# Kernel optimization log

Measured on AMD Instinct MI355X. Metric: run time of the kernel, lower is better.

## Reference

```python
import jax, jax.numpy as jnp
import numpy as np

B, R, SR, K, F = 1, 2048, 24, 8, 32
DIST_FREQ = 2   # dist_xyz_freq -> PE dim 2*2*3 = 12
VIEW_FREQ = 4   # num_viewdir_freqs -> PE dim 2*4*3 = 24


def pe(x, n_freqs):
    # positional encoding: concat sin/cos of x * 2^i, flattened over last dim
    fb = (2.0 ** jnp.arange(n_freqs)).astype(x.dtype)          # [L]
    xb = x[..., None] * fb                                      # [..., 3, L]
    enc = jnp.concatenate([jnp.sin(xb), jnp.cos(xb)], axis=-1)  # [..., 3, 2L]
    return enc.reshape(*x.shape[:-1], -1)                       # [..., 3*2L]


def setup_inputs() -> dict:
    key = jax.random.key(0)
    ks = jax.random.split(key, 12)
    s = 0.1  # small init scale for weights
    return {
        'sampled_embedding': jax.random.normal(ks[0], (B, R, SR, K, F), jnp.float32),
        'dists': jax.random.normal(ks[1], (B, R, SR, K, 3), jnp.float32) * 0.1,
        'viewdirs': jax.random.normal(ks[2], (B, R, SR, 3), jnp.float32),
        'pnt_mask': jax.random.randint(ks[3], (B, R, SR, K), 0, 2, jnp.int32),
        'w1': jax.random.normal(ks[4], (F + 2 * DIST_FREQ * 3, 256), jnp.float32) * s,
        'b1': jnp.zeros((256,), jnp.float32),
        'w2': jax.random.normal(ks[5], (256, 256), jnp.float32) * s,
        'b2': jnp.zeros((256,), jnp.float32),
        'wa1': jax.random.normal(ks[6], (256, 256), jnp.float32) * s,
        'ba1': jnp.zeros((256,), jnp.float32),
        'wa2': jax.random.normal(ks[7], (256, 1), jnp.float32) * s,
        'ba2': jnp.zeros((1,), jnp.float32),
        'wc1': jax.random.normal(ks[8], (256 + 2 * VIEW_FREQ * 3, 256), jnp.float32) * s,
        'bc1': jnp.zeros((256,), jnp.float32),
        'wc2': jax.random.normal(ks[9], (256, 3), jnp.float32) * s,
        'bc2': jnp.zeros((3,), jnp.float32),
    }


def reference(sampled_embedding, dists, viewdirs, pnt_mask,
              w1, b1, w2, b2, wa1, ba1, wa2, ba2, wc1, bc1, wc2, bc2):
    mask = pnt_mask.astype(sampled_embedding.dtype)             # [B,R,SR,K]

    # quadric distance kernel -> normalized neighbor weights
    d2 = jnp.sum(dists * dists, axis=-1)                        # [B,R,SR,K]
    w = 1.0 / jnp.clip(d2, 1e-8)
    w = w * mask
    w = w / jnp.clip(jnp.sum(w, axis=-1, keepdims=True), 1e-8)  # agg_weight_norm

    # per-neighbor feature MLP (block1): feat ++ PE(dist_xyz) -> 256 -> 256
    feat_in = jnp.concatenate([sampled_embedding, pe(dists, DIST_FREQ)], axis=-1)
    h = jax.nn.relu(feat_in @ w1 + b1)
    h = jax.nn.relu(h @ w2 + b2)                                # [B,R,SR,K,256]

    # distance-weighted aggregation over neighbors (apply_pnt_mask folded into w)
    agg = jnp.einsum('brsk,brskc->brsc', w, h)                  # [B,R,SR,256]

    # alpha branch + raw2out_density (act_super: softplus(raw - 1))
    ah = jax.nn.relu(agg @ wa1 + ba1)
    density = jax.nn.softplus(ah @ wa2 + ba2 - 1.0)             # [B,R,SR,1]

    # color branch + raw2out_color (widened sigmoid)
    cin = jnp.concatenate([agg, pe(viewdirs, VIEW_FREQ)], axis=-1)
    ch = jax.nn.relu(cin @ wc1 + bc1)
    color = jax.nn.sigmoid(ch @ wc2 + bc2) * (1.0 + 2e-3) - 1e-3  # [B,R,SR,3]

    return jnp.concatenate([density, color], axis=-1)           # [B,R,SR,4]
```

## Files before the change

### kernel.cpp

```cpp
#include <hip/hip_runtime.h>

typedef unsigned short ushort_t;
typedef __bf16 bf16x8 __attribute__((ext_vector_type(8)));
typedef float f32x4 __attribute__((ext_vector_type(4)));

#define NPTS   49152
#define KNBR   8
#define PTS_A  16
#define NBLK_A (NPTS / PTS_A)
#define PTS_B  32
#define NBLK_B (NPTS / PTS_B)

#define W1S_OFF   0
#define W2S_OFF   16384
#define WA1S_OFF  81920
#define WC1S_OFF  147456
#define WA2S_OFF  221184
#define WC2S_OFF  225280
#define WS_WEIGHT 229376
#define AGG_OFF   229376

__device__ __forceinline__ float b2f(ushort_t u) {
    return __builtin_bit_cast(float, ((unsigned)u) << 16);
}
__device__ __forceinline__ ushort_t f2b(float f) {
    unsigned x = __builtin_bit_cast(unsigned, f);
    unsigned r = x + 0x7fffu + ((x >> 16) & 1u);
    return (ushort_t)(r >> 16);
}
__device__ __forceinline__ ushort_t f2bc(float f) {
    unsigned x = __builtin_bit_cast(unsigned, f);
    return (ushort_t)((x + 0x8000u) >> 16);
}

__global__ __launch_bounds__(256) void prep_swizzle(
    const float* __restrict__ w1, const float* __restrict__ w2,
    const float* __restrict__ wa1, const float* __restrict__ wc1,
    const float* __restrict__ wa2, const float* __restrict__ wc2,
    ushort_t* __restrict__ ws)
{
    int idx = blockIdx.x * 256 + threadIdx.x;
    if (idx >= WS_WEIGHT) return;

    if (idx >= WA2S_OFF) {
        int off2 = idx - WA2S_OFF;
        int mat = off2 >> 12;
        int off = off2 & 4095;
        int kb = off >> 7, rem = off & 127;
        int n = rem >> 3, j = rem & 7;
        int k = kb * 8 + j;
        float v = 0.f;
        if (mat == 0) { if (n == 0) v = wa2[k]; }
        else          { if (n < 3)  v = wc2[k * 3 + n]; }
        ws[idx] = f2b(v);
        return;
    }

    const float* src; int off, srcK, base;
    if (idx < W2S_OFF)        { src = w1;  base = W1S_OFF;  off = idx - W1S_OFF;  srcK = 44;  }
    else if (idx < WA1S_OFF)  { src = w2;  base = W2S_OFF;  off = idx - W2S_OFF;  srcK = 256; }
    else if (idx < WC1S_OFF)  { src = wa1; base = WA1S_OFF; off = idx - WA1S_OFF; srcK = 256; }
    else                      { src = wc1; base = WC1S_OFF; off = idx - WC1S_OFF; srcK = 280; }
    int kb  = off >> 11;
    int rem = off & 2047;
    int j = rem >> 8;
    int n = rem & 255;
    int k = kb * 8 + j;
    float v = (k < srcK) ? src[k * 256 + n] : 0.f;
    ws[base + kb * 2048 + n * 8 + j] = f2b(v);
}

__global__ __launch_bounds__(512, 4) void pa_mlp(
    const float* __restrict__ emb, const float* __restrict__ dists,
    const int* __restrict__ mask,  const float* __restrict__ b1,
    const float* __restrict__ b2,  const ushort_t* __restrict__ ws,
    ushort_t* __restrict__ aggg)
{
    __shared__ __align__(16) ushort_t uH1[128 * 264];
    __shared__ __align__(16) float sWraw[128];
    __shared__ __align__(16) float sWn[128];
    ushort_t (*sFeat)[72] = (ushort_t(*)[72])uH1;
    ushort_t (*sH1)[264]  = (ushort_t(*)[264])uH1;

    const int tid  = threadIdx.x;
    const int lane = tid & 63;
    const int wv   = tid >> 6;
    const int wm   = wv >> 2;
    const int wn   = wv & 3;
    const int n0   = lane & 15;
    const int quad = lane >> 4;
    const int pb   = blockIdx.x * PTS_A;
    const int rowB = wm * 64;
    const int colB = wn * 64;

    {
        int g0 = blockIdx.x * 4096 + tid * 8;
        int r = tid >> 2, c8 = (tid & 3) * 8;
        float4 f0 = *(const float4*)(emb + g0);
        float4 f1 = *(const float4*)(emb + g0 + 4);
        ushort_t v8[8];
        v8[0] = f2bc(f0.x); v8[1] = f2bc(f0.y); v8[2] = f2bc(f0.z); v8[3] = f2bc(f0.w);
        v8[4] = f2bc(f1.x); v8[5] = f2bc(f1.y); v8[6] = f2bc(f1.z); v8[7] = f2bc(f1.w);
        *(uint4*)&sFeat[r][c8] = *(uint4*)v8;
    }
    if (tid < 128) {
        int gr = pb * KNBR + tid;
        float x = dists[gr * 3 + 0];
        float y = dists[gr * 3 + 1];
        float z = dists[gr * 3 + 2];
        float d2 = x * x + y * y + z * z;
        sWraw[tid] = (float)mask[gr] / fmaxf(d2, 1e-8f);
        float xs[3] = {x, y, z};
        #pragma unroll
        for (int d = 0; d < 3; d++) {
            #pragma unroll
            for (int l = 0; l < 2; l++) {
                float ang = xs[d] * (float)(1 << l);
                sFeat[tid][32 + d * 4 + l]     = f2bc(__sinf(ang));
                sFeat[tid][32 + d * 4 + 2 + l] = f2bc(__cosf(ang));
            }
        }
        #pragma unroll
        for (int c = 44; c < 64; c++) sFeat[tid][c] = 0;
    }
    __syncthreads();
    if (tid < 128) {
        int lp = tid >> 3;
        float s = 0.f;
        #pragma unroll
        for (int k = 0; k < 8; k++) s += sWraw[lp * 8 + k];
        sWn[tid] = sWraw[tid] / fmaxf(s, 1e-8f);
    }

    f32x4 acc[16];
    #pragma unroll
    for (int i = 0; i < 16; i++) acc[i] = (f32x4){0.f, 0.f, 0.f, 0.f};

    #pragma unroll
    for (int ki = 0; ki < 2; ki++) {
        bf16x8 a[4];
        #pragma unroll
        for (int mt = 0; mt < 4; mt++)
            a[mt] = *(const bf16x8*)&sFeat[rowB + mt * 16 + n0][ki * 32 + quad * 8];
        const ushort_t* bp = ws + W1S_OFF + ki * 8192 + quad * 2048 + (colB + n0) * 8;
        #pragma unroll
        for (int nt = 0; nt < 4; nt++) {
            bf16x8 b = *(const bf16x8*)(bp + nt * 128);
            #pragma unroll
            for (int mt = 0; mt < 4; mt++)
                acc[mt * 4 + nt] = __builtin_amdgcn_mfma_f32_16x16x32_bf16(a[mt], b, acc[mt * 4 + nt], 0, 0, 0);
        }
    }
    __syncthreads();

    {
        #pragma unroll
        for (int nt = 0; nt < 4; nt++) {
            int col = colB + nt * 16 + n0;
            float bias = b1[col];
            #pragma unroll
            for (int mt = 0; mt < 4; mt++)
                #pragma unroll
                for (int r = 0; r < 4; r++)
                    sH1[rowB + mt * 16 + quad * 4 + r][col] = f2bc(fmaxf(acc[mt * 4 + nt][r] + bias, 0.f));
        }
    }
    __syncthreads();

    #pragma unroll
    for (int i = 0; i < 16; i++) acc[i] = (f32x4){0.f, 0.f, 0.f, 0.f};
    #pragma unroll
    for (int ki = 0; ki < 8; ki++) {
        bf16x8 a[4];
        #pragma unroll
        for (int mt = 0; mt < 4; mt++)
            a[mt] = *(const bf16x8*)&sH1[rowB + mt * 16 + n0][ki * 32 + quad * 8];
        const ushort_t* bp = ws + W2S_OFF + ki * 8192 + quad * 2048 + (colB + n0) * 8;
        #pragma unroll
        for (int nt = 0; nt < 4; nt++) {
            bf16x8 b = *(const bf16x8*)(bp + nt * 128);
            #pragma unroll
            for (int mt = 0; mt < 4; mt++)
                acc[mt * 4 + nt] = __builtin_amdgcn_mfma_f32_16x16x32_bf16(a[mt], b, acc[mt * 4 + nt], 0, 0, 0);
        }
    }
    {
        #pragma unroll
        for (int mt = 0; mt < 4; mt++) {
            f32x4 wn4 = *(const f32x4*)&sWn[rowB + mt * 16 + quad * 4];
            #pragma unroll
            for (int nt = 0; nt < 4; nt++) {
                int col = colB + nt * 16 + n0;
                float bias = b2[col];
                float s = fmaxf(acc[mt * 4 + nt][0] + bias, 0.f) * wn4[0]
                        + fmaxf(acc[mt * 4 + nt][1] + bias, 0.f) * wn4[1]
                        + fmaxf(acc[mt * 4 + nt][2] + bias, 0.f) * wn4[2]
                        + fmaxf(acc[mt * 4 + nt][3] + bias, 0.f) * wn4[3];
                s += __shfl_xor(s, 16);
                if ((quad & 1) == 0) {
                    int pt = pb + 8 * wm + 2 * mt + (quad >> 1);
                    aggg[(size_t)pt * 256 + col] = f2bc(s);
                }
            }
        }
    }
}

__global__ __launch_bounds__(256) void pa_branch(
    const float* __restrict__ vdirs,
    const float* __restrict__ ba1v, const float* __restrict__ ba2v,
    const float* __restrict__ bc1v, const float* __restrict__ bc2v,
    const ushort_t* __restrict__ ws, const ushort_t* __restrict__ aggg,
    float* __restrict__ out)
{
    __shared__ __align__(16) ushort_t reg1[32 * 296];
    __shared__ __align__(16) ushort_t reg2[32 * 264];
    ushort_t (*sCin)[296] = (ushort_t(*)[296])reg1;
    ushort_t (*sAh)[264]  = (ushort_t(*)[264])reg1;
    ushort_t (*sCh)[264]  = (ushort_t(*)[264])reg2;

    const int tid  = threadIdx.x;
    const int lane = tid & 63;
    const int wv   = tid >> 6;
    const int n0   = lane & 15;
    const int quad = lane >> 4;
    const int pb   = blockIdx.x * PTS_B;
    const int colB = wv * 64;

    #pragma unroll
    for (int it = 0; it < 4; it++) {
        int idx = (tid + it * 256) * 8;
        uint4 v = *(const uint4*)(aggg + (size_t)pb * 256 + idx);
        *(uint4*)&sCin[idx >> 8][idx & 255] = v;
    }
    #pragma unroll
    for (int it = 0; it < 3; it++) {
        int t = tid + it * 256;
        int p = t / 24, j = t % 24;
        int d = j >> 3, jj = j & 7, l = jj & 3, isc = jj >> 2;
        float ang = vdirs[(pb + p) * 3 + d] * (float)(1 << l);
        sCin[p][256 + j] = f2bc(isc ? __cosf(ang) : __sinf(ang));
    }
    sCin[tid >> 3][280 + (tid & 7)] = 0;
    __syncthreads();

    f32x4 accA[8], accC[8];
    #pragma unroll
    for (int i = 0; i < 8; i++) { accA[i] = (f32x4){0.f, 0.f, 0.f, 0.f}; accC[i] = accA[i]; }

    #pragma unroll
    for (int ki = 0; ki < 8; ki++) {
        bf16x8 a0 = *(const bf16x8*)&sCin[n0][ki * 32 + quad * 8];
        bf16x8 a1 = *(const bf16x8*)&sCin[16 + n0][ki * 32 + quad * 8];
        const ushort_t* bp = ws + WA1S_OFF + ki * 8192 + quad * 2048 + (colB + n0) * 8;
        #pragma unroll
        for (int nt = 0; nt < 4; nt++) {
            bf16x8 b = *(const bf16x8*)(bp + nt * 128);
            accA[nt]     = __builtin_amdgcn_mfma_f32_16x16x32_bf16(a0, b, accA[nt], 0, 0, 0);
            accA[4 + nt] = __builtin_amdgcn_mfma_f32_16x16x32_bf16(a1, b, accA[4 + nt], 0, 0, 0);
        }
    }
    #pragma unroll
    for (int ki = 0; ki < 9; ki++) {
        bf16x8 a0 = *(const bf16x8*)&sCin[n0][ki * 32 + quad * 8];
        bf16x8 a1 = *(const bf16x8*)&sCin[16 + n0][ki * 32 + quad * 8];
        const ushort_t* bp = ws + WC1S_OFF + ki * 8192 + quad * 2048 + (colB + n0) * 8;
        #pragma unroll
        for (int nt = 0; nt < 4; nt++) {
            bf16x8 b = *(const bf16x8*)(bp + nt * 128);
            accC[nt]     = __builtin_amdgcn_mfma_f32_16x16x32_bf16(a0, b, accC[nt], 0, 0, 0);
            accC[4 + nt] = __builtin_amdgcn_mfma_f32_16x16x32_bf16(a1, b, accC[4 + nt], 0, 0, 0);
        }
    }
    __syncthreads();

    #pragma unroll
    for (int nt = 0; nt < 4; nt++) {
        int col = colB + nt * 16 + n0;
        float biasA = ba1v[col];
        float biasC = bc1v[col];
        #pragma unroll
        for (int mt = 0; mt < 2; mt++)
            #pragma unroll
            for (int r = 0; r < 4; r++) {
                int row = mt * 16 + quad * 4 + r;
                sAh[row][col] = f2bc(fmaxf(accA[mt * 4 + nt][r] + biasA, 0.f));
                sCh[row][col] = f2bc(fmaxf(accC[mt * 4 + nt][r] + biasC, 0.f));
            }
    }
    __syncthreads();

    {
        const int isColor = wv >> 1;
        const int baseM   = (wv & 1) * 16;
        const ushort_t* A = isColor ? &sCh[0][0] : &sAh[0][0];
        const ushort_t* B = ws + (isColor ? WC2S_OFF : WA2S_OFF);
        f32x4 acc4 = (f32x4){0.f, 0.f, 0.f, 0.f};
        #pragma unroll
        for (int ki = 0; ki < 8; ki++) {
            bf16x8 a = *(const bf16x8*)(A + (baseM + n0) * 264 + ki * 32 + quad * 8);
            bf16x8 b = *(const bf16x8*)(B + ki * 512 + quad * 128 + n0 * 8);
            acc4 = __builtin_amdgcn_mfma_f32_16x16x32_bf16(a, b, acc4, 0, 0, 0);
        }
        if (!isColor) {
            if (n0 == 0) {
                float ba2s = ba2v[0];
                #pragma unroll
                for (int r = 0; r < 4; r++) {
                    int gp = pb + baseM + quad * 4 + r;
                    float yv = acc4[r] + ba2s - 1.0f;
                    out[(size_t)gp * 4] = (yv > 20.f) ? yv : log1pf(expf(yv));
                }
            }
        } else {
            if (n0 < 3) {
                float bc2s = bc2v[n0];
                #pragma unroll
                for (int r = 0; r < 4; r++) {
                    int gp = pb + baseM + quad * 4 + r;
                    float sig = 1.f / (1.f + expf(-(acc4[r] + bc2s)));
                    out[(size_t)gp * 4 + 1 + n0] = sig * (1.0f + 2e-3f) - 1e-3f;
                }
            }
        }
    }
}

extern "C" void kernel_launch(void* const* d_in, const int* in_sizes, int n_in,
                              void* d_out, int out_size, void* d_ws, size_t ws_size,
                              hipStream_t stream) {
    const float* emb   = (const float*)d_in[0];
    const float* dists = (const float*)d_in[1];
    const float* vdir  = (const float*)d_in[2];
    const int*   mask  = (const int*)d_in[3];
    const float* w1    = (const float*)d_in[4];
    const float* b1    = (const float*)d_in[5];
    const float* w2    = (const float*)d_in[6];
    const float* b2    = (const float*)d_in[7];
    const float* wa1   = (const float*)d_in[8];
    const float* ba1   = (const float*)d_in[9];
    const float* wa2   = (const float*)d_in[10];
    const float* ba2   = (const float*)d_in[11];
    const float* wc1   = (const float*)d_in[12];
    const float* bc1   = (const float*)d_in[13];
    const float* wc2   = (const float*)d_in[14];
    const float* bc2   = (const float*)d_in[15];
    ushort_t* ws  = (ushort_t*)d_ws;
    float*    out = (float*)d_out;

    prep_swizzle<<<dim3((WS_WEIGHT + 255) / 256), dim3(256), 0, stream>>>(
        w1, w2, wa1, wc1, wa2, wc2, ws);
    pa_mlp<<<dim3(NBLK_A), dim3(512), 0, stream>>>(
        emb, dists, mask, b1, b2, ws, ws + AGG_OFF);
    pa_branch<<<dim3(NBLK_B), dim3(256), 0, stream>>>(
        vdir, ba1, ba2, bc1, bc2, ws, ws + AGG_OFF, out);
}
```

Baseline: 200.3 us.

## Switch MLP matmuls to 32x32x16 MFMA tiles with W2 register prefetch

Both kernels move from 16x16x32 bf16 MFMA to 32x32x16 bf16 MFMA. This halves the number of A/B fragment loads per output and cuts instruction count, and the fragment indexing and epilogue row mapping are rewritten to match the 32x32 accumulator layout. The W2 loop in pa_mlp also double-buffers the global weight fragments in registers so the next k-step's loads overlap the current MFMAs. The trade-off is larger accumulator vectors and more live registers, which could pressure occupancy under launch_bounds(512,4). The weight layout assumption (ki*4096 + hi*2048 stride) must match the preprocessed weight packing.

```diff
diff --git a/kernel.cpp b/kernel.cpp
--- a/kernel.cpp
+++ b/kernel.cpp
@@ -3,6 +3,7 @@
 typedef unsigned short ushort_t;
 typedef __bf16 bf16x8 __attribute__((ext_vector_type(8)));
 typedef float f32x4 __attribute__((ext_vector_type(4)));
+typedef float f32x16 __attribute__((ext_vector_type(16)));
 
 #define NPTS   49152
 #define KNBR   8
@@ -87,8 +88,8 @@
     const int wv   = tid >> 6;
     const int wm   = wv >> 2;
     const int wn   = wv & 3;
-    const int n0   = lane & 15;
-    const int quad = lane >> 4;
+    const int l31  = lane & 31;
+    const int hi   = lane >> 5;
     const int pb   = blockIdx.x * PTS_A;
     const int rowB = wm * 64;
     const int colB = wn * 64;
@@ -132,74 +133,84 @@
         sWn[tid] = sWraw[tid] / fmaxf(s, 1e-8f);
     }
 
-    f32x4 acc[16];
-    #pragma unroll
-    for (int i = 0; i < 16; i++) acc[i] = (f32x4){0.f, 0.f, 0.f, 0.f};
-
-    #pragma unroll
-    for (int ki = 0; ki < 2; ki++) {
-        bf16x8 a[4];
-        #pragma unroll
-        for (int mt = 0; mt < 4; mt++)
-            a[mt] = *(const bf16x8*)&sFeat[rowB + mt * 16 + n0][ki * 32 + quad * 8];
-        const ushort_t* bp = ws + W1S_OFF + ki * 8192 + quad * 2048 + (colB + n0) * 8;
-        #pragma unroll
-        for (int nt = 0; nt < 4; nt++) {
-            bf16x8 b = *(const bf16x8*)(bp + nt * 128);
-            #pragma unroll
-            for (int mt = 0; mt < 4; mt++)
-                acc[mt * 4 + nt] = __builtin_amdgcn_mfma_f32_16x16x32_bf16(a[mt], b, acc[mt * 4 + nt], 0, 0, 0);
-        }
-    }
-    __syncthreads();
-
-    {
-        #pragma unroll
-        for (int nt = 0; nt < 4; nt++) {
-            int col = colB + nt * 16 + n0;
+    f32x16 acc[4];
+    #pragma unroll
+    for (int i = 0; i < 4; i++) acc[i] = (f32x16)(0.f);
+
+    #pragma unroll
+    for (int ki = 0; ki < 4; ki++) {
+        bf16x8 a0 = *(const bf16x8*)&sFeat[rowB + l31][ki * 16 + hi * 8];
+        bf16x8 a1 = *(const bf16x8*)&sFeat[rowB + 32 + l31][ki * 16 + hi * 8];
+        const ushort_t* bp = ws + W1S_OFF + ki * 4096 + hi * 2048 + (colB + l31) * 8;
+        bf16x8 b0 = *(const bf16x8*)(bp);
+        bf16x8 b1f = *(const bf16x8*)(bp + 256);
+        acc[0] = __builtin_amdgcn_mfma_f32_32x32x16_bf16(a0, b0,  acc[0], 0, 0, 0);
+        acc[1] = __builtin_amdgcn_mfma_f32_32x32x16_bf16(a0, b1f, acc[1], 0, 0, 0);
+        acc[2] = __builtin_amdgcn_mfma_f32_32x32x16_bf16(a1, b0,  acc[2], 0, 0, 0);
+        acc[3] = __builtin_amdgcn_mfma_f32_32x32x16_bf16(a1, b1f, acc[3], 0, 0, 0);
+    }
+    __syncthreads();
+
+    {
+        #pragma unroll
+        for (int nt = 0; nt < 2; nt++) {
+            int col = colB + nt * 32 + l31;
             float bias = b1[col];
             #pragma unroll
-            for (int mt = 0; mt < 4; mt++)
+            for (int mt = 0; mt < 2; mt++) {
                 #pragma unroll
-                for (int r = 0; r < 4; r++)
-                    sH1[rowB + mt * 16 + quad * 4 + r][col] = f2bc(fmaxf(acc[mt * 4 + nt][r] + bias, 0.f));
-        }
-    }
-    __syncthreads();
-
-    #pragma unroll
-    for (int i = 0; i < 16; i++) acc[i] = (f32x4){0.f, 0.f, 0.f, 0.f};
-    #pragma unroll
-    for (int ki = 0; ki < 8; ki++) {
-        bf16x8 a[4];
-        #pragma unroll
-        for (int mt = 0; mt < 4; mt++)
-            a[mt] = *(const bf16x8*)&sH1[rowB + mt * 16 + n0][ki * 32 + quad * 8];
-        const ushort_t* bp = ws + W2S_OFF + ki * 8192 + quad * 2048 + (colB + n0) * 8;
-        #pragma unroll
-        for (int nt = 0; nt < 4; nt++) {
-            bf16x8 b = *(const bf16x8*)(bp + nt * 128);
+                for (int reg = 0; reg < 16; reg++) {
+                    int row = rowB + mt * 32 + (reg & 3) + 8 * (reg >> 2) + 4 * hi;
+                    sH1[row][col] = f2bc(fmaxf(acc[mt * 2 + nt][reg] + bias, 0.f));
+                }
+            }
+        }
+    }
+    __syncthreads();
+
+    #pragma unroll
+    for (int i = 0; i < 4; i++) acc[i] = (f32x16)(0.f);
+    {
+        const ushort_t* w2base = ws + W2S_OFF + hi * 2048 + (colB + l31) * 8;
+        bf16x8 bc0 = *(const bf16x8*)(w2base);
+        bf16x8 bc1 = *(const bf16x8*)(w2base + 256);
+        #pragma unroll
+        for (int ki = 0; ki < 16; ki++) {
+            bf16x8 bn0, bn1;
+            if (ki < 15) {
+                const ushort_t* p = w2base + (ki + 1) * 4096;
+                bn0 = *(const bf16x8*)(p);
+                bn1 = *(const bf16x8*)(p + 256);
+            }
+            bf16x8 a0 = *(const bf16x8*)&sH1[rowB + l31][ki * 16 + hi * 8];
+            bf16x8 a1 = *(const bf16x8*)&sH1[rowB + 32 + l31][ki * 16 + hi * 8];
+            acc[0] = __builtin_amdgcn_mfma_f32_32x32x16_bf16(a0, bc0, acc[0], 0, 0, 0);
+            acc[1] = __builtin_amdgcn_mfma_f32_32x32x16_bf16(a0, bc1, acc[1], 0, 0, 0);
+            acc[2] = __builtin_amdgcn_mfma_f32_32x32x16_bf16(a1, bc0, acc[2], 0, 0, 0);
+            acc[3] = __builtin_amdgcn_mfma_f32_32x32x16_bf16(a1, bc1, acc[3], 0, 0, 0);
+            bc0 = bn0; bc1 = bn1;
+        }
+    }
+    {
+        #pragma unroll
+        for (int mt = 0; mt < 2; mt++) {
             #pragma unroll
-            for (int mt = 0; mt < 4; mt++)
-                acc[mt * 4 + nt] = __builtin_amdgcn_mfma_f32_16x16x32_bf16(a[mt], b, acc[mt * 4 + nt], 0, 0, 0);
-        }
-    }
-    {
-        #pragma unroll
-        for (int mt = 0; mt < 4; mt++) {
-            f32x4 wn4 = *(const f32x4*)&sWn[rowB + mt * 16 + quad * 4];
-            #pragma unroll
-            for (int nt = 0; nt < 4; nt++) {
-                int col = colB + nt * 16 + n0;
+            for (int nt = 0; nt < 2; nt++) {
+                int col = colB + nt * 32 + l31;
                 float bias = b2[col];
-                float s = fmaxf(acc[mt * 4 + nt][0] + bias, 0.f) * wn4[0]
-                        + fmaxf(acc[mt * 4 + nt][1] + bias, 0.f) * wn4[1]
-                        + fmaxf(acc[mt * 4 + nt][2] + bias, 0.f) * wn4[2]
-                        + fmaxf(acc[mt * 4 + nt][3] + bias, 0.f) * wn4[3];
-                s += __shfl_xor(s, 16);
-                if ((quad & 1) == 0) {
-                    int pt = pb + 8 * wm + 2 * mt + (quad >> 1);
-                    aggg[(size_t)pt * 256 + col] = f2bc(s);
+                f32x16 v = acc[mt * 2 + nt];
+                #pragma unroll
+                for (int q = 0; q < 4; q++) {
+                    f32x4 wn4 = *(const f32x4*)&sWn[rowB + mt * 32 + q * 8 + 4 * hi];
+                    float s = fmaxf(v[q * 4 + 0] + bias, 0.f) * wn4[0]
+                            + fmaxf(v[q * 4 + 1] + bias, 0.f) * wn4[1]
+                            + fmaxf(v[q * 4 + 2] + bias, 0.f) * wn4[2]
+                            + fmaxf(v[q * 4 + 3] + bias, 0.f) * wn4[3];
+                    s += __shfl_xor(s, 32);
+                    if (hi == 0) {
+                        int pt = pb + wm * 8 + mt * 4 + q;
+                        aggg[(size_t)pt * 256 + col] = f2bc(s);
+                    }
                 }
             }
         }
@@ -222,6 +233,8 @@
     const int tid  = threadIdx.x;
     const int lane = tid & 63;
     const int wv   = tid >> 6;
+    const int l31  = lane & 31;
+    const int hi   = lane >> 5;
     const int n0   = lane & 15;
     const int quad = lane >> 4;
     const int pb   = blockIdx.x * PTS_B;
@@ -244,49 +257,43 @@
     sCin[tid >> 3][280 + (tid & 7)] = 0;
     __syncthreads();
 
-    f32x4 accA[8], accC[8];
-    #pragma unroll
-    for (int i = 0; i < 8; i++) { accA[i] = (f32x4){0.f, 0.f, 0.f, 0.f}; accC[i] = accA[i]; }
-
-    #pragma unroll
-    for (int ki = 0; ki < 8; ki++) {
-        bf16x8 a0 = *(const bf16x8*)&sCin[n0][ki * 32 + quad * 8];
-        bf16x8 a1 = *(const bf16x8*)&sCin[16 + n0][ki * 32 + quad * 8];
-        const ushort_t* bp = ws + WA1S_OFF + ki * 8192 + quad * 2048 + (colB + n0) * 8;
-        #pragma unroll
-        for (int nt = 0; nt < 4; nt++) {
-            bf16x8 b = *(const bf16x8*)(bp + nt * 128);
-            accA[nt]     = __builtin_amdgcn_mfma_f32_16x16x32_bf16(a0, b, accA[nt], 0, 0, 0);
-            accA[4 + nt] = __builtin_amdgcn_mfma_f32_16x16x32_bf16(a1, b, accA[4 + nt], 0, 0, 0);
-        }
-    }
-    #pragma unroll
-    for (int ki = 0; ki < 9; ki++) {
-        bf16x8 a0 = *(const bf16x8*)&sCin[n0][ki * 32 + quad * 8];
-        bf16x8 a1 = *(const bf16x8*)&sCin[16 + n0][ki * 32 + quad * 8];
-        const ushort_t* bp = ws + WC1S_OFF + ki * 8192 + quad * 2048 + (colB + n0) * 8;
-        #pragma unroll
-        for (int nt = 0; nt < 4; nt++) {
-            bf16x8 b = *(const bf16x8*)(bp + nt * 128);
-            accC[nt]     = __builtin_amdgcn_mfma_f32_16x16x32_bf16(a0, b, accC[nt], 0, 0, 0);
-            accC[4 + nt] = __builtin_amdgcn_mfma_f32_16x16x32_bf16(a1, b, accC[4 + nt], 0, 0, 0);
-        }
-    }
-    __syncthreads();
-
-    #pragma unroll
-    for (int nt = 0; nt < 4; nt++) {
-        int col = colB + nt * 16 + n0;
-        float biasA = ba1v[col];
-        float biasC = bc1v[col];
-        #pragma unroll
-        for (int mt = 0; mt < 2; mt++)
+    f32x16 accA[2], accC[2];
+    #pragma unroll
+    for (int i = 0; i < 2; i++) { accA[i] = (f32x16)(0.f); accC[i] = (f32x16)(0.f); }
+
+    #pragma unroll
+    for (int ki = 0; ki < 16; ki++) {
+        bf16x8 a0 = *(const bf16x8*)&sCin[l31][ki * 16 + hi * 8];
+        const ushort_t* bp = ws + WA1S_OFF + ki * 4096 + hi * 2048 + (colB + l31) * 8;
+        bf16x8 b0 = *(const bf16x8*)(bp);
+        bf16x8 b1f = *(const bf16x8*)(bp + 256);
+        accA[0] = __builtin_amdgcn_mfma_f32_32x32x16_bf16(a0, b0,  accA[0], 0, 0, 0);
+        accA[1] = __builtin_amdgcn_mfma_f32_32x32x16_bf16(a0, b1f, accA[1], 0, 0, 0);
+    }
+    #pragma unroll
+    for (int ki = 0; ki < 18; ki++) {
+        bf16x8 a0 = *(const bf16x8*)&sCin[l31][ki * 16 + hi * 8];
+        const ushort_t* bp = ws + WC1S_OFF + ki * 4096 + hi * 2048 + (colB + l31) * 8;
+        bf16x8 b0 = *(const bf16x8*)(bp);
+        bf16x8 b1f = *(const bf16x8*)(bp + 256);
+        accC[0] = __builtin_amdgcn_mfma_f32_32x32x16_bf16(a0, b0,  accC[0], 0, 0, 0);
+        accC[1] = __builtin_amdgcn_mfma_f32_32x32x16_bf16(a0, b1f, accC[1], 0, 0, 0);
+    }
+    __syncthreads();
+
+    {
+        #pragma unroll
+        for (int nt = 0; nt < 2; nt++) {
+            int col = colB + nt * 32 + l31;
+            float biasA = ba1v[col];
+            float biasC = bc1v[col];
             #pragma unroll
-            for (int r = 0; r < 4; r++) {
-                int row = mt * 16 + quad * 4 + r;
-                sAh[row][col] = f2bc(fmaxf(accA[mt * 4 + nt][r] + biasA, 0.f));
-                sCh[row][col] = f2bc(fmaxf(accC[mt * 4 + nt][r] + biasC, 0.f));
-            }
+            for (int reg = 0; reg < 16; reg++) {
+                int row = (reg & 3) + 8 * (reg >> 2) + 4 * hi;
+                sAh[row][col] = f2bc(fmaxf(accA[nt][reg] + biasA, 0.f));
+                sCh[row][col] = f2bc(fmaxf(accC[nt][reg] + biasC, 0.f));
+            }
+        }
     }
     __syncthreads();
 
```

New measurement: 203.8 us. About the same (+1.8%).

## Fuse alpha/color branch MLP into aggregation kernel via shared memory

Applied to the files above, without the earlier changes.

Merges the branch kernel into the per-neighbor MLP kernel so each 16-point block computes aggregated features into LDS and then runs the alpha and color heads directly. This removes the global write and re-read of the bf16 aggregation buffer and one kernel launch. In exchange, each block now does its branch GEMMs with M=16 rows, so branch weights are reloaded from global/L2 per 16 points instead of per 32. It also adds LDS use and extra barriers, which may reduce occupancy.

```diff
diff --git a/kernel.cpp b/kernel.cpp
--- a/kernel.cpp
+++ b/kernel.cpp
@@ -8,8 +8,6 @@
 #define KNBR   8
 #define PTS_A  16
 #define NBLK_A (NPTS / PTS_A)
-#define PTS_B  32
-#define NBLK_B (NPTS / PTS_B)
 
 #define W1S_OFF   0
 #define W2S_OFF   16384
@@ -18,7 +16,6 @@
 #define WA2S_OFF  221184
 #define WC2S_OFF  225280
 #define WS_WEIGHT 229376
-#define AGG_OFF   229376
 
 __device__ __forceinline__ float b2f(ushort_t u) {
     return __builtin_bit_cast(float, ((unsigned)u) << 16);
@@ -72,15 +69,21 @@
 
 __global__ __launch_bounds__(512, 4) void pa_mlp(
     const float* __restrict__ emb, const float* __restrict__ dists,
-    const int* __restrict__ mask,  const float* __restrict__ b1,
-    const float* __restrict__ b2,  const ushort_t* __restrict__ ws,
-    ushort_t* __restrict__ aggg)
+    const int* __restrict__ mask,  const float* __restrict__ vdirs,
+    const float* __restrict__ b1,  const float* __restrict__ b2,
+    const float* __restrict__ ba1v, const float* __restrict__ ba2v,
+    const float* __restrict__ bc1v, const float* __restrict__ bc2v,
+    const ushort_t* __restrict__ ws, float* __restrict__ out)
 {
     __shared__ __align__(16) ushort_t uH1[128 * 264];
     __shared__ __align__(16) float sWraw[128];
     __shared__ __align__(16) float sWn[128];
+    __shared__ __align__(16) ushort_t uCin[16 * 296];
     ushort_t (*sFeat)[72] = (ushort_t(*)[72])uH1;
     ushort_t (*sH1)[264]  = (ushort_t(*)[264])uH1;
+    ushort_t (*sAh)[264]  = (ushort_t(*)[264])uH1;
+    ushort_t (*sCh)[264]  = (ushort_t(*)[264])(uH1 + 16 * 264);
+    ushort_t (*sCi)[296]  = (ushort_t(*)[296])uCin;
 
     const int tid  = threadIdx.x;
     const int lane = tid & 63;
@@ -122,6 +125,13 @@
         }
         #pragma unroll
         for (int c = 44; c < 64; c++) sFeat[tid][c] = 0;
+        sCi[tid >> 3][280 + (tid & 7)] = 0;
+    }
+    if (tid < 384) {
+        int p = tid / 24, j = tid % 24;
+        int d = j >> 3, jj = j & 7, l = jj & 3, isc = jj >> 2;
+        float ang = vdirs[(pb + p) * 3 + d] * (float)(1 << l);
+        sCi[p][256 + j] = f2bc(isc ? __cosf(ang) : __sinf(ang));
     }
     __syncthreads();
     if (tid < 128) {
@@ -198,107 +208,61 @@
                         + fmaxf(acc[mt * 4 + nt][3] + bias, 0.f) * wn4[3];
                 s += __shfl_xor(s, 16);
                 if ((quad & 1) == 0) {
-                    int pt = pb + 8 * wm + 2 * mt + (quad >> 1);
-                    aggg[(size_t)pt * 256 + col] = f2bc(s);
+                    int ptl = 8 * wm + 2 * mt + (quad >> 1);
+                    sCi[ptl][col] = f2bc(s);
                 }
             }
         }
     }
-}
-
-__global__ __launch_bounds__(256) void pa_branch(
-    const float* __restrict__ vdirs,
-    const float* __restrict__ ba1v, const float* __restrict__ ba2v,
-    const float* __restrict__ bc1v, const float* __restrict__ bc2v,
-    const ushort_t* __restrict__ ws, const ushort_t* __restrict__ aggg,
-    float* __restrict__ out)
-{
-    __shared__ __align__(16) ushort_t reg1[32 * 296];
-    __shared__ __align__(16) ushort_t reg2[32 * 264];
-    ushort_t (*sCin)[296] = (ushort_t(*)[296])reg1;
-    ushort_t (*sAh)[264]  = (ushort_t(*)[264])reg1;
-    ushort_t (*sCh)[264]  = (ushort_t(*)[264])reg2;
-
-    const int tid  = threadIdx.x;
-    const int lane = tid & 63;
-    const int wv   = tid >> 6;
-    const int n0   = lane & 15;
-    const int quad = lane >> 4;
-    const int pb   = blockIdx.x * PTS_B;
-    const int colB = wv * 64;
-
-    #pragma unroll
-    for (int it = 0; it < 4; it++) {
-        int idx = (tid + it * 256) * 8;
-        uint4 v = *(const uint4*)(aggg + (size_t)pb * 256 + idx);
-        *(uint4*)&sCin[idx >> 8][idx & 255] = v;
-    }
-    #pragma unroll
-    for (int it = 0; it < 3; it++) {
-        int t = tid + it * 256;
-        int p = t / 24, j = t % 24;
-        int d = j >> 3, jj = j & 7, l = jj & 3, isc = jj >> 2;
-        float ang = vdirs[(pb + p) * 3 + d] * (float)(1 << l);
-        sCin[p][256 + j] = f2bc(isc ? __cosf(ang) : __sinf(ang));
-    }
-    sCin[tid >> 3][280 + (tid & 7)] = 0;
-    __syncthreads();
-
-    f32x4 accA[8], accC[8];
-    #pragma unroll
-    for (int i = 0; i < 8; i++) { accA[i] = (f32x4){0.f, 0.f, 0.f, 0.f}; accC[i] = accA[i]; }
-
-    #pragma unroll
-    for (int ki = 0; ki < 8; ki++) {
-        bf16x8 a0 = *(const bf16x8*)&sCin[n0][ki * 32 + quad * 8];
-        bf16x8 a1 = *(const bf16x8*)&sCin[16 + n0][ki * 32 + quad * 8];
-        const ushort_t* bp = ws + WA1S_OFF + ki * 8192 + quad * 2048 + (colB + n0) * 8;
+    __syncthreads();
+
+    {
+        const int isColor = wv >> 2;
+        const int colBb   = (wv & 3) * 64;
+        const ushort_t* Wb = ws + (isColor ? WC1S_OFF : WA1S_OFF);
+        const float* biasv = isColor ? bc1v : ba1v;
+        f32x4 accB[4];
+        #pragma unroll
+        for (int i = 0; i < 4; i++) accB[i] = (f32x4){0.f, 0.f, 0.f, 0.f};
+        #pragma unroll
+        for (int ki = 0; ki < 8; ki++) {
+            bf16x8 a0 = *(const bf16x8*)&sCi[n0][ki * 32 + quad * 8];
+            const ushort_t* bp = Wb + ki * 8192 + quad * 2048 + (colBb + n0) * 8;
+            #pragma unroll
+            for (int nt = 0; nt < 4; nt++) {
+                bf16x8 b = *(const bf16x8*)(bp + nt * 128);
+                accB[nt] = __builtin_amdgcn_mfma_f32_16x16x32_bf16(a0, b, accB[nt], 0, 0, 0);
+            }
+        }
+        if (isColor) {
+            bf16x8 a0 = *(const bf16x8*)&sCi[n0][8 * 32 + quad * 8];
+            const ushort_t* bp = Wb + 8 * 8192 + quad * 2048 + (colBb + n0) * 8;
+            #pragma unroll
+            for (int nt = 0; nt < 4; nt++) {
+                bf16x8 b = *(const bf16x8*)(bp + nt * 128);
+                accB[nt] = __builtin_amdgcn_mfma_f32_16x16x32_bf16(a0, b, accB[nt], 0, 0, 0);
+            }
+        }
+        ushort_t (*sOut)[264] = isColor ? sCh : sAh;
         #pragma unroll
         for (int nt = 0; nt < 4; nt++) {
-            bf16x8 b = *(const bf16x8*)(bp + nt * 128);
-            accA[nt]     = __builtin_amdgcn_mfma_f32_16x16x32_bf16(a0, b, accA[nt], 0, 0, 0);
-            accA[4 + nt] = __builtin_amdgcn_mfma_f32_16x16x32_bf16(a1, b, accA[4 + nt], 0, 0, 0);
-        }
-    }
-    #pragma unroll
-    for (int ki = 0; ki < 9; ki++) {
-        bf16x8 a0 = *(const bf16x8*)&sCin[n0][ki * 32 + quad * 8];
-        bf16x8 a1 = *(const bf16x8*)&sCin[16 + n0][ki * 32 + quad * 8];
-        const ushort_t* bp = ws + WC1S_OFF + ki * 8192 + quad * 2048 + (colB + n0) * 8;
-        #pragma unroll
-        for (int nt = 0; nt < 4; nt++) {
-            bf16x8 b = *(const bf16x8*)(bp + nt * 128);
-            accC[nt]     = __builtin_amdgcn_mfma_f32_16x16x32_bf16(a0, b, accC[nt], 0, 0, 0);
-            accC[4 + nt] = __builtin_amdgcn_mfma_f32_16x16x32_bf16(a1, b, accC[4 + nt], 0, 0, 0);
-        }
-    }
-    __syncthreads();
-
-    #pragma unroll
-    for (int nt = 0; nt < 4; nt++) {
-        int col = colB + nt * 16 + n0;
-        float biasA = ba1v[col];
-        float biasC = bc1v[col];
-        #pragma unroll
-        for (int mt = 0; mt < 2; mt++)
-            #pragma unroll
-            for (int r = 0; r < 4; r++) {
-                int row = mt * 16 + quad * 4 + r;
-                sAh[row][col] = f2bc(fmaxf(accA[mt * 4 + nt][r] + biasA, 0.f));
-                sCh[row][col] = f2bc(fmaxf(accC[mt * 4 + nt][r] + biasC, 0.f));
-            }
-    }
-    __syncthreads();
-
-    {
-        const int isColor = wv >> 1;
-        const int baseM   = (wv & 1) * 16;
+            int col = colBb + nt * 16 + n0;
+            float bias = biasv[col];
+            #pragma unroll
+            for (int r = 0; r < 4; r++)
+                sOut[quad * 4 + r][col] = f2bc(fmaxf(accB[nt][r] + bias, 0.f));
+        }
+    }
+    __syncthreads();
+
+    if (wv < 2) {
+        const int isColor = wv;
         const ushort_t* A = isColor ? &sCh[0][0] : &sAh[0][0];
         const ushort_t* B = ws + (isColor ? WC2S_OFF : WA2S_OFF);
         f32x4 acc4 = (f32x4){0.f, 0.f, 0.f, 0.f};
         #pragma unroll
         for (int ki = 0; ki < 8; ki++) {
-            bf16x8 a = *(const bf16x8*)(A + (baseM + n0) * 264 + ki * 32 + quad * 8);
+            bf16x8 a = *(const bf16x8*)(A + n0 * 264 + ki * 32 + quad * 8);
             bf16x8 b = *(const bf16x8*)(B + ki * 512 + quad * 128 + n0 * 8);
             acc4 = __builtin_amdgcn_mfma_f32_16x16x32_bf16(a, b, acc4, 0, 0, 0);
         }
@@ -307,7 +271,7 @@
                 float ba2s = ba2v[0];
                 #pragma unroll
                 for (int r = 0; r < 4; r++) {
-                    int gp = pb + baseM + quad * 4 + r;
+                    int gp = pb + quad * 4 + r;
                     float yv = acc4[r] + ba2s - 1.0f;
                     out[(size_t)gp * 4] = (yv > 20.f) ? yv : log1pf(expf(yv));
                 }
@@ -317,7 +281,7 @@
                 float bc2s = bc2v[n0];
                 #pragma unroll
                 for (int r = 0; r < 4; r++) {
-                    int gp = pb + baseM + quad * 4 + r;
+                    int gp = pb + quad * 4 + r;
                     float sig = 1.f / (1.f + expf(-(acc4[r] + bc2s)));
                     out[(size_t)gp * 4 + 1 + n0] = sig * (1.0f + 2e-3f) - 1e-3f;
                 }
@@ -351,7 +315,5 @@
     prep_swizzle<<<dim3((WS_WEIGHT + 255) / 256), dim3(256), 0, stream>>>(
         w1, w2, wa1, wc1, wa2, wc2, ws);
     pa_mlp<<<dim3(NBLK_A), dim3(512), 0, stream>>>(
-        emb, dists, mask, b1, b2, ws, ws + AGG_OFF);
-    pa_branch<<<dim3(NBLK_B), dim3(256), 0, stream>>>(
-        vdir, ba1, ba2, bc1, bc2, ws, ws + AGG_OFF, out);
-}
+        emb, dists, mask, vdir, b1, b2, ba1, ba2, bc1, bc2, ws, out);
+}
```

New measurement: 217.6 us. 8.6% more time.
